# Kernel tuning notes

Hardware: AMD Instinct MI355X
Metric: run time of the kernel (lower is better)

The kernel has to match this reference:

```python
import jax, jax.numpy as jnp
import numpy as np

BS, NS, NO, REL_DIM, MEM_DIM = 2, 48, 48, 512, 256
LN_EPS = 1e-6


def setup_inputs() -> dict:
    key = jax.random.key(0)
    ks = jax.random.split(key, 4)
    s_in = 1.0 / np.sqrt(REL_DIM)
    s_mem = 1.0 / np.sqrt(MEM_DIM)
    return {
        "rel_reprs": jax.random.normal(ks[0], (BS, NS, NO, REL_DIM), dtype=jnp.float32),
        "W1": jax.random.normal(ks[1], (REL_DIM, MEM_DIM), dtype=jnp.float32) * s_in,
        "b1": jnp.zeros((MEM_DIM,), dtype=jnp.float32),
        "W2": jax.random.normal(ks[2], (REL_DIM, MEM_DIM), dtype=jnp.float32) * s_in,
        "b2": jnp.zeros((MEM_DIM,), dtype=jnp.float32),
        "We": jax.random.normal(ks[3], (MEM_DIM, MEM_DIM), dtype=jnp.float32) * s_mem,
        "be": jnp.zeros((MEM_DIM,), dtype=jnp.float32),
        "gamma": jnp.ones((MEM_DIM,), dtype=jnp.float32),
        "beta": jnp.zeros((MEM_DIM,), dtype=jnp.float32),
    }


def reference(rel_reprs, W1, b1, W2, b2, We, be, gamma, beta):
    # factor_type='sib', factor_encoder='biaf' (factorize=True), eval mode (dropout=identity).
    # Original: ha[b,s,o1,o2,:] = rel_reprs[b,s,o1,:]; hb[b,s,o1,o2,:] = rel_reprs[b,s,o2,:]
    # proj then broadcast (identical math to broadcasting then proj, since linears act on last dim).
    p1 = rel_reprs @ W1 + b1  # [bs, ns, no, mem]
    p2 = rel_reprs @ W2 + b2  # [bs, ns, no, mem]
    prod = p1[:, :, :, None, :] * p2[:, :, None, :, :]  # [bs, ns, no, no, mem]
    h = prod @ We + be  # encoder linear
    # LayerNorm(mem_dim, eps=1e-6)
    mu = jnp.mean(h, axis=-1, keepdims=True)
    var = jnp.mean(jnp.square(h - mu), axis=-1, keepdims=True)
    out = (h - mu) * jax.lax.rsqrt(var + LN_EPS) * gamma + beta
    return out
```

## Files before the change

### kernel.cpp

```cpp
#include <hip/hip_runtime.h>

typedef unsigned short ushort_t;
typedef __attribute__((ext_vector_type(8))) short bf16x8;
typedef __attribute__((ext_vector_type(4))) float f32x4;

#define BS 2
#define NS 48
#define NO 48
#define RD 512
#define MD 256
#define M1 (BS*NS*NO)
#define LN_EPS 1e-6f

__device__ __forceinline__ short f2bf(float f) {
    union { float f; unsigned u; } v; v.f = f;
    unsigned u = v.u;
    return (short)((u + 0x7fffu + ((u >> 16) & 1u)) >> 16);
}
__device__ __forceinline__ short f2bf_fast(float f) {
    union { float f; unsigned u; } v; v.f = f;
    return (short)((v.u + 0x8000u) >> 16);
}

__global__ __launch_bounds__(512) void prep_kernel(
    const float* __restrict__ W1, const float* __restrict__ W2,
    const float* __restrict__ We,
    ushort_t* __restrict__ w1F, ushort_t* __restrict__ w2F,
    ushort_t* __restrict__ weF)
{
    __shared__ float tile[64][65];
    int b = blockIdx.x;
    const float* src; ushort_t* dst; int NKS, kT, nT;
    if (b < 32)      { src = W1; dst = w1F; NKS = 16; kT = b >> 2;        nT = b & 3; }
    else if (b < 64) { src = W2; dst = w2F; NKS = 16; kT = (b - 32) >> 2; nT = b & 3; }
    else             { src = We; dst = weF; NKS = 8;  kT = (b - 64) >> 2; nT = b & 3; }
    int R0 = kT * 64, C0 = nT * 64;
    int tid = threadIdx.x;
#pragma unroll
    for (int pass = 0; pass < 2; ++pass) {
        int kl = pass * 32 + (tid >> 4);
        int nl = (tid & 15) * 4;
        float4 v = *reinterpret_cast<const float4*>(src + (size_t)(R0 + kl) * MD + C0 + nl);
        tile[kl][nl + 0] = v.x; tile[kl][nl + 1] = v.y;
        tile[kl][nl + 2] = v.z; tile[kl][nl + 3] = v.w;
    }
    __syncthreads();
    int f = tid >> 6, lane = tid & 63, lr = lane & 15, lg = lane >> 4;
    int ntl = f >> 1, ksl = f & 1;
    int ntG = (C0 >> 4) + ntl, ksG = (R0 >> 5) + ksl;
    bf16x8 v;
#pragma unroll
    for (int e = 0; e < 8; ++e)
        v[e] = f2bf(tile[ksl * 32 + lg * 8 + e][ntl * 16 + lr]);
    *reinterpret_cast<bf16x8*>(dst + ((size_t)(ntG * NKS + ksG) * 64 + lane) * 8) = v;
}

__global__ __launch_bounds__(256) void stage1_kernel(
    const float* __restrict__ rel,
    const ushort_t* __restrict__ w1F, const ushort_t* __restrict__ w2F,
    const float* __restrict__ b1, const float* __restrict__ b2,
    float* __restrict__ p1, float* __restrict__ p2)
{
    __shared__ __align__(16) char ldsA[16 * RD * 2];
    int blk = blockIdx.x;
    int mt = blk >> 1, which = blk & 1;
    const ushort_t* wF = which ? w2F : w1F;
    const float* bias  = which ? b2 : b1;
    float* out         = which ? p2 : p1;
    int tid = threadIdx.x, wid = tid >> 6, lane = tid & 63;
    int lr = lane & 15, lg = lane >> 4;

#pragma unroll
    for (int it = 0; it < 8; ++it) {
        int rr = it * 2 + (tid >> 7);
        int c  = (tid & 127) * 4;
        float4 v = *reinterpret_cast<const float4*>(rel + (size_t)(mt * 16 + rr) * RD + c);
        short4 s;
        s.x = f2bf_fast(v.x); s.y = f2bf_fast(v.y);
        s.z = f2bf_fast(v.z); s.w = f2bf_fast(v.w);
        *reinterpret_cast<short4*>(ldsA + rr * (RD * 2) + ((c * 2) ^ ((rr & 7) << 4))) = s;
    }
    __syncthreads();

    int n0 = wid * 64;
    f32x4 acc[4] = {};
#pragma unroll
    for (int ks = 0; ks < 16; ++ks) {
        bf16x8 a = *reinterpret_cast<const bf16x8*>(
            ldsA + lr * (RD * 2) + ((ks * 64 + lg * 16) ^ ((lr & 7) << 4)));
#pragma unroll
        for (int nt = 0; nt < 4; ++nt) {
            int ntG = (n0 >> 4) + nt;
            bf16x8 bfr = *reinterpret_cast<const bf16x8*>(
                wF + ((size_t)(ntG * 16 + ks) * 64 + lane) * 8);
            acc[nt] = __builtin_amdgcn_mfma_f32_16x16x32_bf16(a, bfr, acc[nt], 0, 0, 0);
        }
    }
#pragma unroll
    for (int nt = 0; nt < 4; ++nt) {
        int col = n0 + nt * 16 + lr;
        float bv = bias[col];
#pragma unroll
        for (int r = 0; r < 4; ++r) {
            int orow = mt * 16 + lg * 4 + r;
            out[(size_t)orow * MD + col] = acc[nt][r] + bv;
        }
    }
}

__global__ __launch_bounds__(512, 4) void stage2_kernel(
    const float* __restrict__ p1, const float* __restrict__ p2,
    const ushort_t* __restrict__ weF,
    const float* __restrict__ be, const float* __restrict__ gamma,
    const float* __restrict__ beta, float* __restrict__ out)
{
    __shared__ __align__(16) char lds[49152];
    __shared__ float pS1[NO][8];
    __shared__ float pS2[NO][8];
    __shared__ float muS[NO];
    __shared__ float rsS[NO];

    int d    = blockIdx.x;
    int bid  = (d & 7) * 576 + (d >> 3);
    int grp  = (bid / NO) * NO;
    int tid  = threadIdx.x;
    int wid  = tid >> 6;
    int lane = tid & 63;
    int lr   = lane & 15;
    int lg   = lane >> 4;
    int m0w  = wid * 32;

    const float* p1r = p1 + (size_t)bid * MD;
#pragma unroll
    for (int i = 0; i < 6; ++i) {
        int r  = i * 8 + wid;
        int m0 = lane * 4;
        float4 x = *reinterpret_cast<const float4*>(p1r + m0);
        float4 y = *reinterpret_cast<const float4*>(p2 + (size_t)(grp + r) * MD + m0);
        short4 s;
        s.x = f2bf_fast(x.x * y.x); s.y = f2bf_fast(x.y * y.y);
        s.z = f2bf_fast(x.z * y.z); s.w = f2bf_fast(x.w * y.w);
        *reinterpret_cast<short4*>(lds + r * (MD * 2) + ((m0 * 2) ^ ((r & 7) << 4))) = s;
    }

    bf16x8 afrag[2][8];
#pragma unroll
    for (int mt = 0; mt < 2; ++mt) {
        int ntG = (m0w >> 4) + mt;
#pragma unroll
        for (int ks = 0; ks < 8; ++ks)
            afrag[mt][ks] = *reinterpret_cast<const bf16x8*>(
                weF + ((size_t)(ntG * 8 + ks) * 64 + lane) * 8);
    }
    __syncthreads();

    f32x4 acc[2][3] = {};
#pragma unroll
    for (int ks = 0; ks < 8; ++ks) {
        bf16x8 b[3];
#pragma unroll
        for (int nt = 0; nt < 3; ++nt) {
            int r = nt * 16 + lr;
            b[nt] = *reinterpret_cast<const bf16x8*>(
                lds + r * (MD * 2) + ((ks * 64 + lg * 16) ^ ((r & 7) << 4)));
        }
#pragma unroll
        for (int mt = 0; mt < 2; ++mt)
#pragma unroll
            for (int nt = 0; nt < 3; ++nt)
                acc[mt][nt] = __builtin_amdgcn_mfma_f32_16x16x32_bf16(
                    afrag[mt][ks], b[nt], acc[mt][nt], 0, 0, 0);
    }

#pragma unroll
    for (int mt = 0; mt < 2; ++mt) {
        float4 bev = *reinterpret_cast<const float4*>(be + m0w + mt * 16 + lg * 4);
#pragma unroll
        for (int nt = 0; nt < 3; ++nt) {
            acc[mt][nt][0] += bev.x; acc[mt][nt][1] += bev.y;
            acc[mt][nt][2] += bev.z; acc[mt][nt][3] += bev.w;
        }
    }

#pragma unroll
    for (int nt = 0; nt < 3; ++nt) {
        float s1 = 0.f, s2 = 0.f;
#pragma unroll
        for (int mt = 0; mt < 2; ++mt)
#pragma unroll
            for (int r = 0; r < 4; ++r) {
                float v = acc[mt][nt][r];
                s1 += v; s2 += v * v;
            }
        s1 += __shfl_xor(s1, 16); s2 += __shfl_xor(s2, 16);
        s1 += __shfl_xor(s1, 32); s2 += __shfl_xor(s2, 32);
        if (lane < 16) {
            pS1[nt * 16 + lane][wid] = s1;
            pS2[nt * 16 + lane][wid] = s2;
        }
    }
    __syncthreads();

    if (tid < NO) {
        f32x4 a0 = *reinterpret_cast<const f32x4*>(&pS1[tid][0]);
        f32x4 a1 = *reinterpret_cast<const f32x4*>(&pS1[tid][4]);
        f32x4 b0 = *reinterpret_cast<const f32x4*>(&pS2[tid][0]);
        f32x4 b1v = *reinterpret_cast<const f32x4*>(&pS2[tid][4]);
        float S1 = a0[0]+a0[1]+a0[2]+a0[3] + a1[0]+a1[1]+a1[2]+a1[3];
        float S2 = b0[0]+b0[1]+b0[2]+b0[3] + b1v[0]+b1v[1]+b1v[2]+b1v[3];
        float m  = S1 * (1.0f / MD);
        float var = S2 * (1.0f / MD) - m * m;
        muS[tid] = m;
        rsS[tid] = rsqrtf(var + LN_EPS);
    }
    __syncthreads();

    float4 g4[2], b4[2];
#pragma unroll
    for (int mt = 0; mt < 2; ++mt) {
        g4[mt] = *reinterpret_cast<const float4*>(gamma + m0w + mt * 16 + lg * 4);
        b4[mt] = *reinterpret_cast<const float4*>(beta  + m0w + mt * 16 + lg * 4);
    }
#pragma unroll
    for (int nt = 0; nt < 3; ++nt) {
        int r = nt * 16 + lr;
        float mu = muS[r];
        float rs = rsS[r];
#pragma unroll
        for (int mt = 0; mt < 2; ++mt) {
            float4 o;
            o.x = (acc[mt][nt][0] - mu) * rs * g4[mt].x + b4[mt].x;
            o.y = (acc[mt][nt][1] - mu) * rs * g4[mt].y + b4[mt].y;
            o.z = (acc[mt][nt][2] - mu) * rs * g4[mt].z + b4[mt].z;
            o.w = (acc[mt][nt][3] - mu) * rs * g4[mt].w + b4[mt].w;
            int n4 = (m0w + mt * 16 + lg * 4) * 4;
            *reinterpret_cast<float4*>(
                lds + nt * 16384 + lr * 1024 + (n4 ^ ((lr & 7) << 4))) = o;
        }
    }
    __syncthreads();

    size_t ob = (size_t)bid * NO * MD;
#pragma unroll
    for (int nt = 0; nt < 3; ++nt) {
#pragma unroll
        for (int j = 0; j < 2; ++j) {
            int rl = wid * 2 + j;
            float4 o = *reinterpret_cast<const float4*>(
                lds + nt * 16384 + rl * 1024 + ((lane * 16) ^ ((rl & 7) << 4)));
            *reinterpret_cast<float4*>(
                out + ob + (size_t)(nt * 16 + rl) * MD + lane * 4) = o;
        }
    }
}

extern "C" void kernel_launch(void* const* d_in, const int* in_sizes, int n_in,
                              void* d_out, int out_size, void* d_ws, size_t ws_size,
                              hipStream_t stream) {
    const float* rel   = (const float*)d_in[0];
    const float* W1    = (const float*)d_in[1];
    const float* b1    = (const float*)d_in[2];
    const float* W2    = (const float*)d_in[3];
    const float* b2    = (const float*)d_in[4];
    const float* We    = (const float*)d_in[5];
    const float* be    = (const float*)d_in[6];
    const float* gamma = (const float*)d_in[7];
    const float* beta  = (const float*)d_in[8];
    float* out = (float*)d_out;

    char* ws = (char*)d_ws;
    ushort_t* w1F = (ushort_t*)(ws);
    ushort_t* w2F = (ushort_t*)(ws + 524288);
    ushort_t* weF = (ushort_t*)(ws + 1048576);
    float*    p1  = (float*)   (ws + 1179648);
    float*    p2  = (float*)   (ws + 1179648 + 4718592);

    prep_kernel<<<80, 512, 0, stream>>>(W1, W2, We, w1F, w2F, weF);
    stage1_kernel<<<576, 256, 0, stream>>>(rel, w1F, w2F, b1, b2, p1, p2);
    stage2_kernel<<<M1, 512, 0, stream>>>(p1, p2, weF, be, gamma, beta, out);
}
```

Measured before the change: 82.76 us.

## Process two (b,s,o1) rows per stage2 block to reuse We fragments and p2 loads

Each stage2 block now handles two consecutive o1 rows, 96 product rows in total, instead of one. The p2 row loads and the We bf16 fragments are reused across both outputs, and the grid is halved. To limit register pressure, the We fragments are loaded in two halves of K. The output is written back through LDS in two passes, which adds extra syncs. The larger accumulator set (2x6 tiles) may reduce occupancy.

Result: slower. 86.26 us (+4.2%).

```diff
diff --git a/kernel.cpp b/kernel.cpp
--- a/kernel.cpp
+++ b/kernel.cpp
@@ -115,14 +115,15 @@
     const float* __restrict__ beta, float* __restrict__ out)
 {
     __shared__ __align__(16) char lds[49152];
-    __shared__ float pS1[NO][8];
-    __shared__ float pS2[NO][8];
-    __shared__ float muS[NO];
-    __shared__ float rsS[NO];
+    __shared__ float pS1[96][8];
+    __shared__ float pS2[96][8];
+    __shared__ float muS[96];
+    __shared__ float rsS[96];
 
     int d    = blockIdx.x;
-    int bid  = (d & 7) * 576 + (d >> 3);
-    int grp  = (bid / NO) * NO;
+    int L    = (d & 7) * 288 + (d >> 3);
+    int bid0 = L * 2;
+    int grp  = (bid0 / NO) * NO;
     int tid  = threadIdx.x;
     int wid  = tid >> 6;
     int lane = tid & 63;
@@ -130,60 +131,88 @@
     int lg   = lane >> 4;
     int m0w  = wid * 32;
 
-    const float* p1r = p1 + (size_t)bid * MD;
+    float4 pxa = *reinterpret_cast<const float4*>(p1 + (size_t)bid0 * MD + lane * 4);
+    float4 pxb = *reinterpret_cast<const float4*>(p1 + (size_t)(bid0 + 1) * MD + lane * 4);
 #pragma unroll
     for (int i = 0; i < 6; ++i) {
-        int r  = i * 8 + wid;
-        int m0 = lane * 4;
-        float4 x = *reinterpret_cast<const float4*>(p1r + m0);
-        float4 y = *reinterpret_cast<const float4*>(p2 + (size_t)(grp + r) * MD + m0);
-        short4 s;
-        s.x = f2bf_fast(x.x * y.x); s.y = f2bf_fast(x.y * y.y);
-        s.z = f2bf_fast(x.z * y.z); s.w = f2bf_fast(x.w * y.w);
-        *reinterpret_cast<short4*>(lds + r * (MD * 2) + ((m0 * 2) ^ ((r & 7) << 4))) = s;
-    }
-
-    bf16x8 afrag[2][8];
+        int r = i * 8 + wid;
+        float4 y = *reinterpret_cast<const float4*>(p2 + (size_t)(grp + r) * MD + lane * 4);
+        short4 sA, sB;
+        sA.x = f2bf_fast(pxa.x * y.x); sA.y = f2bf_fast(pxa.y * y.y);
+        sA.z = f2bf_fast(pxa.z * y.z); sA.w = f2bf_fast(pxa.w * y.w);
+        sB.x = f2bf_fast(pxb.x * y.x); sB.y = f2bf_fast(pxb.y * y.y);
+        sB.z = f2bf_fast(pxb.z * y.z); sB.w = f2bf_fast(pxb.w * y.w);
+        int swz = (lane * 8) ^ ((r & 7) << 4);
+        *reinterpret_cast<short4*>(lds + r * 512 + swz) = sA;
+        *reinterpret_cast<short4*>(lds + (r + 48) * 512 + swz) = sB;
+    }
+
+    bf16x8 af[2][4];
 #pragma unroll
     for (int mt = 0; mt < 2; ++mt) {
         int ntG = (m0w >> 4) + mt;
 #pragma unroll
-        for (int ks = 0; ks < 8; ++ks)
-            afrag[mt][ks] = *reinterpret_cast<const bf16x8*>(
+        for (int ks = 0; ks < 4; ++ks)
+            af[mt][ks] = *reinterpret_cast<const bf16x8*>(
                 weF + ((size_t)(ntG * 8 + ks) * 64 + lane) * 8);
     }
     __syncthreads();
 
-    f32x4 acc[2][3] = {};
-#pragma unroll
-    for (int ks = 0; ks < 8; ++ks) {
-        bf16x8 b[3];
-#pragma unroll
-        for (int nt = 0; nt < 3; ++nt) {
+    f32x4 acc[2][6] = {};
+#pragma unroll
+    for (int ks = 0; ks < 4; ++ks) {
+        bf16x8 b[6];
+#pragma unroll
+        for (int nt = 0; nt < 6; ++nt) {
             int r = nt * 16 + lr;
             b[nt] = *reinterpret_cast<const bf16x8*>(
-                lds + r * (MD * 2) + ((ks * 64 + lg * 16) ^ ((r & 7) << 4)));
+                lds + r * 512 + ((ks * 64 + lg * 16) ^ ((r & 7) << 4)));
         }
 #pragma unroll
         for (int mt = 0; mt < 2; ++mt)
 #pragma unroll
-            for (int nt = 0; nt < 3; ++nt)
+            for (int nt = 0; nt < 6; ++nt)
                 acc[mt][nt] = __builtin_amdgcn_mfma_f32_16x16x32_bf16(
-                    afrag[mt][ks], b[nt], acc[mt][nt], 0, 0, 0);
+                    af[mt][ks], b[nt], acc[mt][nt], 0, 0, 0);
+    }
+
+#pragma unroll
+    for (int mt = 0; mt < 2; ++mt) {
+        int ntG = (m0w >> 4) + mt;
+#pragma unroll
+        for (int ks = 0; ks < 4; ++ks)
+            af[mt][ks] = *reinterpret_cast<const bf16x8*>(
+                weF + ((size_t)(ntG * 8 + ks + 4) * 64 + lane) * 8);
+    }
+#pragma unroll
+    for (int ks = 0; ks < 4; ++ks) {
+        bf16x8 b[6];
+#pragma unroll
+        for (int nt = 0; nt < 6; ++nt) {
+            int r = nt * 16 + lr;
+            b[nt] = *reinterpret_cast<const bf16x8*>(
+                lds + r * 512 + (((ks + 4) * 64 + lg * 16) ^ ((r & 7) << 4)));
+        }
+#pragma unroll
+        for (int mt = 0; mt < 2; ++mt)
+#pragma unroll
+            for (int nt = 0; nt < 6; ++nt)
+                acc[mt][nt] = __builtin_amdgcn_mfma_f32_16x16x32_bf16(
+                    af[mt][ks], b[nt], acc[mt][nt], 0, 0, 0);
     }
 
 #pragma unroll
     for (int mt = 0; mt < 2; ++mt) {
         float4 bev = *reinterpret_cast<const float4*>(be + m0w + mt * 16 + lg * 4);
 #pragma unroll
-        for (int nt = 0; nt < 3; ++nt) {
+        for (int nt = 0; nt < 6; ++nt) {
             acc[mt][nt][0] += bev.x; acc[mt][nt][1] += bev.y;
             acc[mt][nt][2] += bev.z; acc[mt][nt][3] += bev.w;
         }
     }
 
 #pragma unroll
-    for (int nt = 0; nt < 3; ++nt) {
+    for (int nt = 0; nt < 6; ++nt) {
         float s1 = 0.f, s2 = 0.f;
 #pragma unroll
         for (int mt = 0; mt < 2; ++mt)
@@ -201,7 +230,7 @@
     }
     __syncthreads();
 
-    if (tid < NO) {
+    if (tid < 96) {
         f32x4 a0 = *reinterpret_cast<const f32x4*>(&pS1[tid][0]);
         f32x4 a1 = *reinterpret_cast<const f32x4*>(&pS1[tid][4]);
         f32x4 b0 = *reinterpret_cast<const f32x4*>(&pS2[tid][0]);
@@ -221,36 +250,40 @@
         g4[mt] = *reinterpret_cast<const float4*>(gamma + m0w + mt * 16 + lg * 4);
         b4[mt] = *reinterpret_cast<const float4*>(beta  + m0w + mt * 16 + lg * 4);
     }
-#pragma unroll
-    for (int nt = 0; nt < 3; ++nt) {
-        int r = nt * 16 + lr;
-        float mu = muS[r];
-        float rs = rsS[r];
-#pragma unroll
-        for (int mt = 0; mt < 2; ++mt) {
-            float4 o;
-            o.x = (acc[mt][nt][0] - mu) * rs * g4[mt].x + b4[mt].x;
-            o.y = (acc[mt][nt][1] - mu) * rs * g4[mt].y + b4[mt].y;
-            o.z = (acc[mt][nt][2] - mu) * rs * g4[mt].z + b4[mt].z;
-            o.w = (acc[mt][nt][3] - mu) * rs * g4[mt].w + b4[mt].w;
-            int n4 = (m0w + mt * 16 + lg * 4) * 4;
-            *reinterpret_cast<float4*>(
-                lds + nt * 16384 + lr * 1024 + (n4 ^ ((lr & 7) << 4))) = o;
-        }
-    }
-    __syncthreads();
-
-    size_t ob = (size_t)bid * NO * MD;
-#pragma unroll
-    for (int nt = 0; nt < 3; ++nt) {
-#pragma unroll
-        for (int j = 0; j < 2; ++j) {
-            int rl = wid * 2 + j;
-            float4 o = *reinterpret_cast<const float4*>(
-                lds + nt * 16384 + rl * 1024 + ((lane * 16) ^ ((rl & 7) << 4)));
-            *reinterpret_cast<float4*>(
-                out + ob + (size_t)(nt * 16 + rl) * MD + lane * 4) = o;
-        }
+    size_t ob0 = (size_t)bid0 * NO * MD;
+#pragma unroll
+    for (int p = 0; p < 2; ++p) {
+#pragma unroll
+        for (int nt = 0; nt < 3; ++nt) {
+            int ra = (p * 3 + nt) * 16 + lr;
+            float mu = muS[ra];
+            float rs = rsS[ra];
+#pragma unroll
+            for (int mt = 0; mt < 2; ++mt) {
+                float4 o;
+                o.x = (acc[mt][p * 3 + nt][0] - mu) * rs * g4[mt].x + b4[mt].x;
+                o.y = (acc[mt][p * 3 + nt][1] - mu) * rs * g4[mt].y + b4[mt].y;
+                o.z = (acc[mt][p * 3 + nt][2] - mu) * rs * g4[mt].z + b4[mt].z;
+                o.w = (acc[mt][p * 3 + nt][3] - mu) * rs * g4[mt].w + b4[mt].w;
+                int n4 = (m0w + mt * 16 + lg * 4) * 4;
+                *reinterpret_cast<float4*>(
+                    lds + nt * 16384 + lr * 1024 + (n4 ^ ((lr & 7) << 4))) = o;
+            }
+        }
+        __syncthreads();
+#pragma unroll
+        for (int nt = 0; nt < 3; ++nt) {
+#pragma unroll
+            for (int j = 0; j < 2; ++j) {
+                int rl = wid * 2 + j;
+                float4 o = *reinterpret_cast<const float4*>(
+                    lds + nt * 16384 + rl * 1024 + ((lane * 16) ^ ((rl & 7) << 4)));
+                *reinterpret_cast<float4*>(
+                    out + ob0 + (size_t)p * NO * MD +
+                    (size_t)(nt * 16 + rl) * MD + lane * 4) = o;
+            }
+        }
+        __syncthreads();
     }
 }
 
@@ -277,5 +310,5 @@
 
     prep_kernel<<<80, 512, 0, stream>>>(W1, W2, We, w1F, w2F, weF);
     stage1_kernel<<<576, 256, 0, stream>>>(rel, w1F, w2F, b1, b2, p1, p2);
-    stage2_kernel<<<M1, 512, 0, stream>>>(p1, p2, weF, be, gamma, beta, out);
-}
+    stage2_kernel<<<2304, 512, 0, stream>>>(p1, p2, weF, be, gamma, beta, out);
+}
```
